# Performance work log

Measured on AMD Instinct MI355X. Metric: run time of the kernel, lower is better.

The kernel has to match this reference:

```python
import jax, jax.numpy as jnp
import numpy as np

B, N, K = 8, 1024, 1024
C1, C2 = 64, 128
EPS = 1e-5
XTOL = 1e-7


def _skew(w):
    x, y, z = w[..., 0], w[..., 1], w[..., 2]
    o = jnp.zeros_like(x)
    r0 = jnp.stack([o, -z, y], axis=-1)
    r1 = jnp.stack([z, o, -x], axis=-1)
    r2 = jnp.stack([-y, x, o], axis=-1)
    return jnp.stack([r0, r1, r2], axis=-2)


def _expmap(dx):
    # se(3) exponential map, twist = [w(3), v(3)] -> [B,4,4]
    w, v = dx[:, :3], dx[:, 3:]
    t = jnp.linalg.norm(w, axis=1)
    W = _skew(w)
    S = jnp.matmul(W, W)
    t2 = t * t
    small = t < 1e-4
    ts = jnp.where(small, jnp.ones_like(t), t)
    s1 = jnp.where(small, 1.0 - t2 / 6.0, jnp.sin(ts) / ts)            # sin(t)/t
    s2 = jnp.where(small, 0.5 - t2 / 24.0, (1.0 - jnp.cos(ts)) / (ts * ts))  # (1-cos t)/t^2
    s3 = jnp.where(small, 1.0 / 6.0 - t2 / 120.0, (ts - jnp.sin(ts)) / (ts * ts * ts))  # (t-sin t)/t^3
    I = jnp.eye(3, dtype=dx.dtype)
    R = I + s1[:, None, None] * W + s2[:, None, None] * S
    V = I + s2[:, None, None] * W + s3[:, None, None] * S
    p = jnp.einsum('bij,bj->bi', V, v)
    g = jnp.zeros((dx.shape[0], 4, 4), dtype=dx.dtype)
    g = g.at[:, :3, :3].set(R).at[:, :3, 3].set(p).at[:, 3, 3].set(1.0)
    return g


def _transform(g, p):
    # g: [B,4,4] rigid transforms, p: [B,N,3]
    return jnp.einsum('bij,bnj->bni', g[:, :3, :3], p) + g[:, None, :3, 3]


def _bn_eval(x, gamma, beta, rm, rv_):
    # eval-mode batchnorm over channel dim of [B,C,N]
    return gamma[:, None] * (x - rm[:, None]) * jax.lax.rsqrt(rv_[:, None] + EPS) + beta[:, None]


def _pointnet(p, params, with_jac=False):
    # shared-MLP PointNet: conv1x1 -> BN(eval) -> ReLU (x3), then max-pool over points
    x = jnp.swapaxes(p, 1, 2)  # [B,3,N]
    masks = []
    for (Wt, b, gamma, beta, rm, rv_) in params:
        x = jnp.einsum('oc,bcn->bon', Wt, x) + b[:, None]
        x = _bn_eval(x, gamma, beta, rm, rv_)
        x = jnp.maximum(x, 0.0)
        if with_jac:
            masks.append((x > 0.0).astype(x.dtype))
    f = jnp.max(x, axis=-1)  # [B,K]
    if with_jac:
        return f, masks, jnp.argmax(x, axis=-1)  # max_idx [B,K]
    return f


def _cal_pinv(p0, params, masks, max_idx):
    # analytical Jacobian (Cal_Jac) + Gauss-Newton pseudo-inverse
    bsz, npts = p0.shape[0], p0.shape[1]
    W1, W2, W3 = params[0][0], params[1][0], params[2][0]
    d1 = params[0][2] * jax.lax.rsqrt(params[0][5] + EPS)  # dBN/dx in eval mode (per channel)
    d2 = params[1][2] * jax.lax.rsqrt(params[1][5] + EPS)
    d3 = params[2][2] * jax.lax.rsqrt(params[2][5] + EPS)
    D1 = d1[None, :, None] * masks[0]  # [B,C1,N]
    D2 = d2[None, :, None] * masks[1]  # [B,C2,N]
    D3 = d3[None, :, None] * masks[2]  # [B,K,N]
    # feature jacobian chain d f / d p : [B,K,N,3]
    t1 = jnp.einsum('ci,bcn->bnic', W1, D1)            # [B,N,3,C1]
    t2 = jnp.einsum('bnic,dc,bdn->bnid', t1, W2, D2)   # [B,N,3,C2]
    fj = jnp.einsum('bnid,kd,bkn->bkni', t2, W3, D3)   # [B,K,N,3]
    # warp jacobian at identity twist: [-[p]x | -I3] -> [B,N,3,6]
    eye3 = jnp.broadcast_to(jnp.eye(3, dtype=p0.dtype), (bsz, npts, 3, 3))
    warp = jnp.concatenate([-_skew(p0), -eye3], axis=-1)
    # gather the argmax point per feature channel (only rows surviving max-pool)
    fjg = jnp.take_along_axis(fj, max_idx[:, :, None, None], axis=2)[:, :, 0, :]  # [B,K,3]
    wg = jnp.take_along_axis(warp.reshape(bsz, npts, 18), max_idx[:, :, None], axis=1)
    wg = wg.reshape(bsz, -1, 3, 6)  # [B,K,3,6]
    J = jnp.einsum('bki,bkim->bkm', fjg, wg)  # [B,K,6]
    H = jnp.einsum('bki,bkj->bij', J, J)      # [B,6,6]
    pinv = jnp.einsum('bij,bkj->bik', jnp.linalg.inv(H), J)  # [B,6,K]
    return pinv


def _forward(p0, p1, W1, b1, gamma1, beta1, rm1, rv1, W2, b2, gamma2, beta2, rm2, rv2, W3, b3, gamma3, beta3, rm3, rv3, maxiter):
    params = [(W1, b1, gamma1, beta1, rm1, rv1),
              (W2, b2, gamma2, beta2, rm2, rv2),
              (W3, b3, gamma3, beta3, rm3, rv3)]
    f0, masks, max_idx = _pointnet(p0, params, with_jac=True)
    pinv = _cal_pinv(p0, params, masks, max_idx)
    bsz = p0.shape[0]
    g0 = jnp.broadcast_to(jnp.eye(4, dtype=p0.dtype), (bsz, 4, 4))

    def step(carry, _):
        g, r, done = carry
        p = _transform(g, p1)
        f = _pointnet(p, params)
        r_new = jnp.where(done, r, f - f0)           # freeze residual after xtol break
        dx = jnp.einsum('bik,bk->bi', pinv, r_new)   # Gauss-Newton step [B,6]
        conv = jnp.max(jnp.linalg.norm(dx, axis=1)) < XTOL
        stop = done | conv
        g_new = jnp.where(stop, g, jnp.matmul(_expmap(dx), g))
        return (g_new, r_new, stop), None

    init = (g0, jnp.zeros_like(f0), jnp.array(False))
    (g, r, _), _ = jax.lax.scan(step, init, None, length=maxiter)
    return r


def setup_inputs():
    key = jax.random.key(0)
    ks = jax.random.split(key, 24)
    f32 = jnp.float32
    rn = lambda i, s, sc=1.0: jax.random.normal(ks[i], s, dtype=f32) * sc
    ru = lambda i, s: jax.random.uniform(ks[i], s, dtype=f32, minval=0.5, maxval=1.5)
    p0 = rn(0, (B, N, 3))
    inp = {
        'p0': p0,
        'p1': p0 + rn(1, (B, N, 3), 0.02),  # small rigid-ish perturbation -> meaningful registration
        'W1': rn(2, (C1, 3), 0.5), 'b1': rn(3, (C1,), 0.1),
        'gamma1': ru(4, (C1,)), 'beta1': rn(5, (C1,), 0.1),
        'rm1': rn(6, (C1,), 0.1), 'rv1': ru(7, (C1,)),
        'W2': rn(8, (C2, C1), 0.2), 'b2': rn(9, (C2,), 0.1),
        'gamma2': ru(10, (C2,)), 'beta2': rn(11, (C2,), 0.1),
        'rm2': rn(12, (C2,), 0.1), 'rv2': ru(13, (C2,)),
        'W3': rn(14, (K, C2), 0.1), 'b3': rn(15, (K,), 0.1),
        'gamma3': ru(16, (K,)), 'beta3': rn(17, (K,), 0.1),
        'rm3': rn(18, (K,), 0.1), 'rv3': ru(19, (K,)),
        'maxiter': 10,
    }
    return inp


def reference(p0, p1, W1, b1, gamma1, beta1, rm1, rv1, W2, b2, gamma2, beta2, rm2, rv2, W3, b3, gamma3, beta3, rm3, rv3, maxiter):
    return _forward(p0, p1, W1, b1, gamma1, beta1, rm1, rv1, W2, b2, gamma2, beta2, rm2, rv2, W3, b3, gamma3, beta3, rm3, rv3, maxiter)
```

## Files before the change

### kernel.cpp

```cpp
#include <hip/hip_runtime.h>

#define B_ 8
#define N_ 1024
#define C1_ 64
#define C2_ 128
#define K_ 1024
#define EPS_ 1e-5f
#define XTOL_ 1e-7f

#define OFF_G      0
#define OFF_F0     128
#define OFF_PM     8320
#define OFF_M1     24704
#define OFF_M2     41088
#define OFF_SC3    73856
#define OFF_OFF3   74880
#define OFF_OFF2   75904
#define OFF_W1F    76032
#define OFF_W3HI   76288
#define OFF_W3LO   141824
#define OFF_W2H    207360
#define OFF_W2L    211456
#define OFF_J      215552
#define OFF_PINVT  264704
#define OFF_PART   330240

typedef __attribute__((ext_vector_type(8))) short bf16x8;
typedef __attribute__((ext_vector_type(4))) float f32x4;

static __device__ inline unsigned short f2bf(float x) {
    unsigned u = __float_as_uint(x);
    unsigned r = (u + 0x7FFFu + ((u >> 16) & 1u)) >> 16;
    return (unsigned short)r;
}
static __device__ inline float bf2f(unsigned short h) {
    return __uint_as_float(((unsigned)h) << 16);
}
static __device__ inline unsigned pk2(unsigned short a, unsigned short b) {
    return (unsigned)a | ((unsigned)b << 16);
}

__global__ __launch_bounds__(256)
void k_prep(const float* __restrict__ W3, const float* __restrict__ b3,
            const float* __restrict__ ga3, const float* __restrict__ be3,
            const float* __restrict__ rm3, const float* __restrict__ rv3,
            const float* __restrict__ W1, const float* __restrict__ b1,
            const float* __restrict__ ga1, const float* __restrict__ be1,
            const float* __restrict__ rm1, const float* __restrict__ rv1,
            const float* __restrict__ W2, const float* __restrict__ b2,
            const float* __restrict__ ga2, const float* __restrict__ be2,
            const float* __restrict__ rm2, const float* __restrict__ rv2,
            unsigned short* __restrict__ w3hi, unsigned short* __restrict__ w3lo,
            float* __restrict__ sc3, float* __restrict__ off3,
            unsigned short* __restrict__ w2h, unsigned short* __restrict__ w2l,
            float* __restrict__ off2, float* __restrict__ w1f) {
    int gid = blockIdx.x * 256 + threadIdx.x;
    if (gid < K_ * C2_) {
        float w = W3[gid];
        unsigned short h = f2bf(w);
        w3hi[gid] = h;
        w3lo[gid] = f2bf(w - bf2f(h));
    }
    if (gid < K_) {
        float sc = ga3[gid] * rsqrtf(rv3[gid] + EPS_);
        sc3[gid] = sc;
        off3[gid] = sc * (b3[gid] - rm3[gid]) + be3[gid];
    }
    if (gid < C2_ * C1_) {
        int o = gid >> 6, c = gid & 63;
        float sc = ga2[o] * rsqrtf(rv2[o] + EPS_);
        float v = W2[o * C1_ + c] * sc;
        unsigned short h = f2bf(v);
        w2h[o * C1_ + c] = h;
        w2l[o * C1_ + c] = f2bf(v - bf2f(h));
    }
    if (gid < C2_) {
        float sc = ga2[gid] * rsqrtf(rv2[gid] + EPS_);
        off2[gid] = sc * (b2[gid] - rm2[gid]) + be2[gid];
    }
    if (gid < C1_) {
        float sc = ga1[gid] * rsqrtf(rv1[gid] + EPS_);
        w1f[gid * 4 + 0] = W1[gid * 3 + 0] * sc;
        w1f[gid * 4 + 1] = W1[gid * 3 + 1] * sc;
        w1f[gid * 4 + 2] = W1[gid * 3 + 2] * sc;
        w1f[gid * 4 + 3] = sc * (b1[gid] - rm1[gid]) + be1[gid];
    }
}

template<int MODE>
__global__ __launch_bounds__(512, 2)
void k_fused(const float* __restrict__ pts, const float* __restrict__ g,
             const float* __restrict__ w1f,
             const unsigned short* __restrict__ w2h, const unsigned short* __restrict__ w2l,
             const float* __restrict__ off2,
             const unsigned short* __restrict__ w3hi, const unsigned short* __restrict__ w3lo,
             const float* __restrict__ sc3, const float* __restrict__ off3,
             unsigned long long* __restrict__ part,
             unsigned long long* __restrict__ m1b, unsigned int* __restrict__ m2q) {
    __shared__ __align__(16) unsigned short a1h[128][72];
    __shared__ __align__(16) unsigned short a1l[128][72];
    __shared__ __align__(16) unsigned short sB[2][128][136];
    __shared__ float sSc[256], sOff[256], sOff2[C2_];
    __shared__ unsigned int m1w[2][128];
    __shared__ unsigned int m2w[4][128];
    __shared__ unsigned long long pmL[256];

    int slab = blockIdx.x;
    int b    = blockIdx.y;
    int q    = blockIdx.z;
    int n0   = slab * 128;
    int tx   = threadIdx.x;
    int w    = tx >> 6;
    int l    = tx & 63;
    int l15  = l & 15;
    int lhi  = l >> 4;

    if (tx < 256) { sSc[tx] = sc3[q * 256 + tx]; sOff[tx] = off3[q * 256 + tx]; }
    if (tx < C2_) sOff2[tx] = off2[tx];
    if (MODE == 0 && tx < 128) {
        m1w[0][tx] = 0u; m1w[1][tx] = 0u;
        m2w[0][tx] = 0u; m2w[1][tx] = 0u; m2w[2][tx] = 0u; m2w[3][tx] = 0u;
    }
    __syncthreads();

    {
        int n = tx & 127;
        int cgi = tx >> 7;
        const float* pp = pts + (b * N_ + n0 + n) * 3;
        float px = pp[0], py = pp[1], pz = pp[2];
        float q0, q1, q2;
        if (MODE == 1) {
            const float* gb = g + b * 16;
            q0 = fmaf(gb[0], px, fmaf(gb[1], py, fmaf(gb[2],  pz, gb[3])));
            q1 = fmaf(gb[4], px, fmaf(gb[5], py, fmaf(gb[6],  pz, gb[7])));
            q2 = fmaf(gb[8], px, fmaf(gb[9], py, fmaf(gb[10], pz, gb[11])));
        } else {
            q0 = px; q1 = py; q2 = pz;
        }
        unsigned int bits = 0u;
        unsigned hw[8], lw[8];
        #pragma unroll
        for (int j = 0; j < 16; ++j) {
            int c = cgi * 16 + j;
            float4 wf = *(const float4*)(w1f + c * 4);
            float y = fmaxf(fmaf(wf.x, q0, fmaf(wf.y, q1, fmaf(wf.z, q2, wf.w))), 0.f);
            unsigned short h = f2bf(y);
            unsigned short lo = f2bf(y - bf2f(h));
            if (j & 1) { hw[j >> 1] |= ((unsigned)h) << 16; lw[j >> 1] |= ((unsigned)lo) << 16; }
            else       { hw[j >> 1] = (unsigned)h;          lw[j >> 1] = (unsigned)lo; }
            if (MODE == 0) bits |= ((unsigned int)(y > 0.f)) << j;
        }
        uint4 v0; v0.x = hw[0]; v0.y = hw[1]; v0.z = hw[2]; v0.w = hw[3];
        uint4 v1; v1.x = hw[4]; v1.y = hw[5]; v1.z = hw[6]; v1.w = hw[7];
        *(uint4*)&a1h[n][cgi * 16 + 0] = v0;
        *(uint4*)&a1h[n][cgi * 16 + 8] = v1;
        uint4 v2; v2.x = lw[0]; v2.y = lw[1]; v2.z = lw[2]; v2.w = lw[3];
        uint4 v3; v3.x = lw[4]; v3.y = lw[5]; v3.z = lw[6]; v3.w = lw[7];
        *(uint4*)&a1l[n][cgi * 16 + 0] = v2;
        *(uint4*)&a1l[n][cgi * 16 + 8] = v3;
        if (MODE == 0) atomicOr(&m1w[cgi >> 1][n], bits << ((cgi & 1) * 16));
    }
    __syncthreads();

    {
        f32x4 acc2[8];
        #pragma unroll
        for (int nf = 0; nf < 8; ++nf) acc2[nf] = (f32x4){0.f, 0.f, 0.f, 0.f};
        #pragma unroll
        for (int ks = 0; ks < 2; ++ks) {
            int k0 = ks * 32;
            int aoff = (w * 16 + l15) * C1_ + k0 + lhi * 8;
            bf16x8 ah2 = *(const bf16x8*)(w2h + aoff);
            bf16x8 al2 = *(const bf16x8*)(w2l + aoff);
            #pragma unroll
            for (int nf = 0; nf < 8; ++nf) {
                bf16x8 bh2 = *(const bf16x8*)&a1h[nf * 16 + l15][k0 + lhi * 8];
                bf16x8 bl2 = *(const bf16x8*)&a1l[nf * 16 + l15][k0 + lhi * 8];
                acc2[nf] = __builtin_amdgcn_mfma_f32_16x16x32_bf16(ah2, bh2, acc2[nf], 0, 0, 0);
                acc2[nf] = __builtin_amdgcn_mfma_f32_16x16x32_bf16(ah2, bl2, acc2[nf], 0, 0, 0);
                acc2[nf] = __builtin_amdgcn_mfma_f32_16x16x32_bf16(al2, bh2, acc2[nf], 0, 0, 0);
            }
        }
        #pragma unroll
        for (int nf = 0; nf < 8; ++nf) {
            int n = nf * 16 + l15;
            unsigned short h4[4], l4[4];
            #pragma unroll
            for (int r = 0; r < 4; ++r) {
                int o = w * 16 + lhi * 4 + r;
                float y = fmaxf(acc2[nf][r] + sOff2[o], 0.f);
                unsigned short h = f2bf(y);
                h4[r] = h;
                l4[r] = f2bf(y - bf2f(h));
                if (MODE == 0 && y > 0.f) atomicOr(&m2w[o >> 5][n], 1u << (o & 31));
            }
            uint2 vh; vh.x = pk2(h4[0], h4[1]); vh.y = pk2(h4[2], h4[3]);
            uint2 vl; vl.x = pk2(l4[0], l4[1]); vl.y = pk2(l4[2], l4[3]);
            *(uint2*)&sB[0][n][w * 16 + lhi * 4] = vh;
            *(uint2*)&sB[1][n][w * 16 + lhi * 4] = vl;
        }
    }
    __syncthreads();

    if (MODE == 0 && q == 0 && tx < 128) {
        m1b[b * N_ + n0 + tx] =
            (unsigned long long)m1w[0][tx] | ((unsigned long long)m1w[1][tx] << 32);
        uint4 mv; mv.x = m2w[0][tx]; mv.y = m2w[1][tx]; mv.z = m2w[2][tx]; mv.w = m2w[3][tx];
        *(uint4*)&m2q[(b * N_ + n0 + tx) * 4] = mv;
    }

    f32x4 acc[2][8];
    #pragma unroll
    for (int fi = 0; fi < 2; ++fi)
        #pragma unroll
        for (int nf = 0; nf < 8; ++nf) acc[fi][nf] = (f32x4){0.f, 0.f, 0.f, 0.f};

    #pragma unroll
    for (int ks = 0; ks < 4; ++ks) {
        int k0 = ks * 32;
        bf16x8 bh[8], bl[8];
        #pragma unroll
        for (int nf = 0; nf < 8; ++nf) {
            bh[nf] = *(const bf16x8*)&sB[0][nf * 16 + l15][k0 + lhi * 8];
            bl[nf] = *(const bf16x8*)&sB[1][nf * 16 + l15][k0 + lhi * 8];
        }
        #pragma unroll
        for (int fi = 0; fi < 2; ++fi) {
            int orow = q * 256 + w * 32 + fi * 16 + l15;
            int off = orow * C2_ + k0 + lhi * 8;
            bf16x8 ah = *(const bf16x8*)(w3hi + off);
            bf16x8 al = *(const bf16x8*)(w3lo + off);
            #pragma unroll
            for (int nf = 0; nf < 8; ++nf) {
                acc[fi][nf] = __builtin_amdgcn_mfma_f32_16x16x32_bf16(ah, bh[nf], acc[fi][nf], 0, 0, 0);
                acc[fi][nf] = __builtin_amdgcn_mfma_f32_16x16x32_bf16(ah, bl[nf], acc[fi][nf], 0, 0, 0);
                acc[fi][nf] = __builtin_amdgcn_mfma_f32_16x16x32_bf16(al, bh[nf], acc[fi][nf], 0, 0, 0);
            }
        }
    }

    #pragma unroll
    for (int fi = 0; fi < 2; ++fi) {
        #pragma unroll
        for (int r = 0; r < 4; ++r) {
            int o_l = w * 32 + fi * 16 + lhi * 4 + r;
            float sc = sSc[o_l], of = sOff[o_l];
            float bv = -3.4e38f;
            int bi = 0;
            #pragma unroll
            for (int nf = 0; nf < 8; ++nf) {
                float y = fmaxf(sc * acc[fi][nf][r] + of, 0.f);
                int nn = n0 + nf * 16 + l15;
                if (y > bv) { bv = y; bi = nn; }
            }
            #pragma unroll
            for (int m = 1; m <= 8; m <<= 1) {
                float ov = __shfl_xor(bv, m);
                int oi = __shfl_xor(bi, m);
                if (ov > bv || (ov == bv && oi < bi)) { bv = ov; bi = oi; }
            }
            if (l15 == 0) {
                pmL[o_l] = ((unsigned long long)__float_as_uint(bv) << 32)
                         | (unsigned int)(~(unsigned int)bi);
            }
        }
    }
    __syncthreads();
    if (tx < 256)
        part[(size_t)slab * (B_ * K_) + b * K_ + q * 256 + tx] = pmL[tx];
}

__global__ __launch_bounds__(256)
void k_reduce(const unsigned long long* __restrict__ part,
              unsigned long long* __restrict__ pm) {
    int gid = blockIdx.x * 256 + threadIdx.x;
    unsigned long long m = part[gid];
    #pragma unroll
    for (int s = 1; s < 8; ++s) {
        unsigned long long v = part[(size_t)s * (B_ * K_) + gid];
        m = (v > m) ? v : m;
    }
    pm[gid] = m;
}

__global__ void k_dxupd(const unsigned long long* __restrict__ pm,
                        const float* __restrict__ f0,
                        const float* __restrict__ pinvT,
                        float* __restrict__ out, float* __restrict__ g) {
    __shared__ float dxs[B_][6];
    __shared__ float nrm[B_];
    __shared__ int sconv;
    int tx = threadIdx.x;
    int w = tx >> 6;
    int l = tx & 63;
    float acc[6] = {0.f, 0.f, 0.f, 0.f, 0.f, 0.f};
    for (int kk = l; kk < K_; kk += 64) {
        unsigned long long pk = pm[w * K_ + kk];
        float fv = __uint_as_float((unsigned int)(pk >> 32));
        float rv_ = fv - f0[w * K_ + kk];
        out[w * K_ + kk] = rv_;
        const float4* pp = (const float4*)(pinvT + (w * K_ + kk) * 8);
        float4 pa = pp[0], pb = pp[1];
        acc[0] += pa.x * rv_; acc[1] += pa.y * rv_; acc[2] += pa.z * rv_;
        acc[3] += pa.w * rv_; acc[4] += pb.x * rv_; acc[5] += pb.y * rv_;
    }
    #pragma unroll
    for (int i = 0; i < 6; ++i)
        for (int off = 32; off > 0; off >>= 1) acc[i] += __shfl_down(acc[i], off);
    if (l == 0) {
        #pragma unroll
        for (int i = 0; i < 6; ++i) dxs[w][i] = acc[i];
        nrm[w] = sqrtf(acc[0]*acc[0] + acc[1]*acc[1] + acc[2]*acc[2]
                     + acc[3]*acc[3] + acc[4]*acc[4] + acc[5]*acc[5]);
    }
    __syncthreads();
    if (tx == 0) {
        float m = nrm[0];
        for (int i = 1; i < B_; ++i) m = fmaxf(m, nrm[i]);
        sconv = (m < XTOL_) ? 1 : 0;
    }
    __syncthreads();
    if (sconv) return;
    if (l == 0) {
        float wx = dxs[w][0], wy = dxs[w][1], wz = dxs[w][2];
        float vx = dxs[w][3], vy = dxs[w][4], vz = dxs[w][5];
        float t2 = wx*wx + wy*wy + wz*wz;
        float t = sqrtf(t2);
        float s1, s2, s3;
        if (t < 1e-4f) {
            s1 = 1.f - t2 / 6.f;
            s2 = 0.5f - t2 / 24.f;
            s3 = 1.f / 6.f - t2 / 120.f;
        } else {
            float st = sinf(t), ct = cosf(t);
            s1 = st / t;
            s2 = (1.f - ct) / t2;
            s3 = (t - st) / (t2 * t);
        }
        float W[3][3] = {{0.f, -wz, wy}, {wz, 0.f, -wx}, {-wy, wx, 0.f}};
        float S[3][3];
        #pragma unroll
        for (int i = 0; i < 3; ++i)
            #pragma unroll
            for (int j = 0; j < 3; ++j)
                S[i][j] = W[i][0]*W[0][j] + W[i][1]*W[1][j] + W[i][2]*W[2][j];
        float R[3][3], V[3][3];
        #pragma unroll
        for (int i = 0; i < 3; ++i)
            #pragma unroll
            for (int j = 0; j < 3; ++j) {
                float id = (i == j) ? 1.f : 0.f;
                R[i][j] = id + s1 * W[i][j] + s2 * S[i][j];
                V[i][j] = id + s2 * W[i][j] + s3 * S[i][j];
            }
        float p[3];
        #pragma unroll
        for (int i = 0; i < 3; ++i) p[i] = V[i][0]*vx + V[i][1]*vy + V[i][2]*vz;
        float* gb = g + w * 16;
        float go[16];
        #pragma unroll
        for (int i = 0; i < 16; ++i) go[i] = gb[i];
        #pragma unroll
        for (int i = 0; i < 3; ++i)
            #pragma unroll
            for (int j = 0; j < 4; ++j)
                gb[i * 4 + j] = R[i][0]*go[0*4+j] + R[i][1]*go[1*4+j]
                              + R[i][2]*go[2*4+j] + p[i]*go[3*4+j];
    }
}

__global__ __launch_bounds__(256)
void k_jac(const float* __restrict__ p0,
           const unsigned long long* __restrict__ m1b,
           const unsigned int* __restrict__ m2q,
           const float* __restrict__ W1, const float* __restrict__ ga1, const float* __restrict__ rv1,
           const float* __restrict__ W2, const float* __restrict__ ga2, const float* __restrict__ rv2,
           const float* __restrict__ W3, const float* __restrict__ ga3, const float* __restrict__ rv3,
           const unsigned long long* __restrict__ pm,
           float* __restrict__ f0, float* __restrict__ J) {
    __shared__ float wvs[4][128];
    int tx = threadIdx.x;
    int wv = tx >> 6;
    int l = tx & 63;
    int w = blockIdx.x * 4 + wv;
    int b = w >> 10;
    int k = w & 1023;

    unsigned long long pk = pm[b * K_ + k];
    float f0v = __uint_as_float((unsigned int)(pk >> 32));
    int ns = (int)(~(unsigned int)pk);
    if (l == 0) f0[b * K_ + k] = f0v;

    unsigned long long m1 = m1b[b * N_ + ns];
    const unsigned int* mq = m2q + (b * N_ + ns) * 4;
    unsigned int qa = mq[0], qb = mq[1], qc = mq[2], qd = mq[3];
    unsigned int blo = (l < 32) ? (qa >> l) : (qb >> (l - 32));
    unsigned int bhi = (l < 32) ? (qc >> l) : (qd >> (l - 32));

    const float* w3r = W3 + k * C2_;
    float s2a = ga2[l] * rsqrtf(rv2[l] + EPS_);
    float s2b = ga2[64 + l] * rsqrtf(rv2[64 + l] + EPS_);
    float wa = (blo & 1u) ? w3r[l] * s2a : 0.f;
    float wb = (bhi & 1u) ? w3r[64 + l] * s2b : 0.f;
    wvs[wv][l] = wa;
    wvs[wv][64 + l] = wb;
    __syncthreads();

    float v = 0.f;
    #pragma unroll 8
    for (int d = 0; d < C2_; ++d) v += wvs[wv][d] * W2[d * C1_ + l];

    float d1l = ((m1 >> l) & 1ull) ? ga1[l] * rsqrtf(rv1[l] + EPS_) : 0.f;
    float vc = v * d1l;
    float fj0 = vc * W1[l * 3 + 0];
    float fj1 = vc * W1[l * 3 + 1];
    float fj2 = vc * W1[l * 3 + 2];
    #pragma unroll
    for (int off = 32; off; off >>= 1) {
        fj0 += __shfl_xor(fj0, off);
        fj1 += __shfl_xor(fj1, off);
        fj2 += __shfl_xor(fj2, off);
    }
    if (l == 0) {
        float D3 = (f0v > 0.f) ? ga3[k] * rsqrtf(rv3[k] + EPS_) : 0.f;
        fj0 *= D3; fj1 *= D3; fj2 *= D3;
        float x = p0[(b * N_ + ns) * 3 + 0];
        float y = p0[(b * N_ + ns) * 3 + 1];
        float z = p0[(b * N_ + ns) * 3 + 2];
        float* Jr = J + (b * K_ + k) * 6;
        Jr[0] = fj1 * (-z) + fj2 * y;
        Jr[1] = fj0 * z    + fj2 * (-x);
        Jr[2] = fj0 * (-y) + fj1 * x;
        Jr[3] = -fj0;
        Jr[4] = -fj1;
        Jr[5] = -fj2;
    }
}

__global__ void k_hpinv(const float* __restrict__ J, float* __restrict__ pinvT,
                        float* __restrict__ g) {
    int b = blockIdx.x;
    int tx = threadIdx.x;
    __shared__ float red[256][22];
    __shared__ float hinv[36];

    if (tx < 16) g[b * 16 + tx] = (tx % 5 == 0) ? 1.f : 0.f;

    float h[21];
    #pragma unroll
    for (int q = 0; q < 21; ++q) h[q] = 0.f;
    for (int k = tx; k < K_; k += 256) {
        const float* Jr = J + (b * K_ + k) * 6;
        float jv[6] = {Jr[0], Jr[1], Jr[2], Jr[3], Jr[4], Jr[5]};
        int q = 0;
        #pragma unroll
        for (int i = 0; i < 6; ++i)
            #pragma unroll
            for (int jj = i; jj < 6; ++jj) h[q++] += jv[i] * jv[jj];
    }
    #pragma unroll
    for (int q = 0; q < 21; ++q) red[tx][q] = h[q];
    __syncthreads();
    for (int s = 128; s > 0; s >>= 1) {
        if (tx < s)
            for (int q = 0; q < 21; ++q) red[tx][q] += red[tx + s][q];
        __syncthreads();
    }
    if (tx == 0) {
        float A[6][6], Inv[6][6];
        {
            int q = 0;
            #pragma unroll
            for (int i = 0; i < 6; ++i)
                #pragma unroll
                for (int jj = i; jj < 6; ++jj) { A[i][jj] = red[0][q]; A[jj][i] = red[0][q]; ++q; }
        }
        #pragma unroll
        for (int i = 0; i < 6; ++i)
            #pragma unroll
            for (int jj = 0; jj < 6; ++jj) Inv[i][jj] = (i == jj) ? 1.f : 0.f;
        #pragma unroll
        for (int col = 0; col < 6; ++col) {
            float ipv = 1.f / A[col][col];
            #pragma unroll
            for (int jj = 0; jj < 6; ++jj) { A[col][jj] *= ipv; Inv[col][jj] *= ipv; }
            #pragma unroll
            for (int r2 = 0; r2 < 6; ++r2) {
                if (r2 == col) continue;
                float f = A[r2][col];
                #pragma unroll
                for (int jj = 0; jj < 6; ++jj) {
                    A[r2][jj]   -= f * A[col][jj];
                    Inv[r2][jj] -= f * Inv[col][jj];
                }
            }
        }
        #pragma unroll
        for (int i = 0; i < 6; ++i)
            #pragma unroll
            for (int jj = 0; jj < 6; ++jj) hinv[i * 6 + jj] = Inv[i][jj];
    }
    __syncthreads();
    for (int k = tx; k < K_; k += 256) {
        const float* Jr = J + (b * K_ + k) * 6;
        float j0 = Jr[0], j1 = Jr[1], j2 = Jr[2], j3 = Jr[3], j4 = Jr[4], j5 = Jr[5];
        float* pr = pinvT + (b * K_ + k) * 8;
        #pragma unroll
        for (int i = 0; i < 6; ++i) {
            pr[i] = hinv[i * 6 + 0] * j0 + hinv[i * 6 + 1] * j1 + hinv[i * 6 + 2] * j2
                  + hinv[i * 6 + 3] * j3 + hinv[i * 6 + 4] * j4 + hinv[i * 6 + 5] * j5;
        }
        pr[6] = 0.f; pr[7] = 0.f;
    }
}

extern "C" void kernel_launch(void* const* d_in, const int* in_sizes, int n_in,
                              void* d_out, int out_size, void* d_ws, size_t ws_size,
                              hipStream_t stream) {
    const float* p0  = (const float*)d_in[0];
    const float* p1  = (const float*)d_in[1];
    const float* W1  = (const float*)d_in[2];
    const float* b1  = (const float*)d_in[3];
    const float* ga1 = (const float*)d_in[4];
    const float* be1 = (const float*)d_in[5];
    const float* rm1 = (const float*)d_in[6];
    const float* rv1 = (const float*)d_in[7];
    const float* W2  = (const float*)d_in[8];
    const float* b2  = (const float*)d_in[9];
    const float* ga2 = (const float*)d_in[10];
    const float* be2 = (const float*)d_in[11];
    const float* rm2 = (const float*)d_in[12];
    const float* rv2 = (const float*)d_in[13];
    const float* W3  = (const float*)d_in[14];
    const float* b3  = (const float*)d_in[15];
    const float* ga3 = (const float*)d_in[16];
    const float* be3 = (const float*)d_in[17];
    const float* rm3 = (const float*)d_in[18];
    const float* rv3 = (const float*)d_in[19];

    float* ws   = (float*)d_ws;
    float* g    = ws + OFF_G;
    float* f0   = ws + OFF_F0;
    unsigned long long* pm  = (unsigned long long*)(ws + OFF_PM);
    unsigned long long* m1b = (unsigned long long*)(ws + OFF_M1);
    unsigned int*       m2q = (unsigned int*)(ws + OFF_M2);
    float* sc3  = ws + OFF_SC3;
    float* off3 = ws + OFF_OFF3;
    float* off2 = ws + OFF_OFF2;
    float* w1f  = ws + OFF_W1F;
    unsigned short* w3hi = (unsigned short*)(ws + OFF_W3HI);
    unsigned short* w3lo = (unsigned short*)(ws + OFF_W3LO);
    unsigned short* w2h  = (unsigned short*)(ws + OFF_W2H);
    unsigned short* w2l  = (unsigned short*)(ws + OFF_W2L);
    float* Jb    = ws + OFF_J;
    float* pinvT = ws + OFF_PINVT;
    unsigned long long* part = (unsigned long long*)(ws + OFF_PART);
    float* out   = (float*)d_out;

    dim3 gridF(8, B_, 4);

    k_prep<<<(K_ * C2_ + 255) / 256, 256, 0, stream>>>(
        W3, b3, ga3, be3, rm3, rv3,
        W1, b1, ga1, be1, rm1, rv1,
        W2, b2, ga2, be2, rm2, rv2,
        w3hi, w3lo, sc3, off3, w2h, w2l, off2, w1f);

    k_fused<0><<<gridF, 512, 0, stream>>>(p0, g, w1f, w2h, w2l, off2, w3hi, w3lo,
                                          sc3, off3, part, m1b, m2q);
    k_reduce<<<B_ * K_ / 256, 256, 0, stream>>>(part, pm);
    k_jac<<<B_ * K_ / 4, 256, 0, stream>>>(p0, m1b, m2q, W1, ga1, rv1, W2, ga2, rv2,
                                           W3, ga3, rv3, pm, f0, Jb);
    k_hpinv<<<B_, 256, 0, stream>>>(Jb, pinvT, g);

    for (int it = 0; it < 10; ++it) {
        k_fused<1><<<gridF, 512, 0, stream>>>(p1, g, w1f, w2h, w2l, off2, w3hi, w3lo,
                                              sc3, off3, part, m1b, m2q);
        k_reduce<<<B_ * K_ / 256, 256, 0, stream>>>(part, pm);
        k_dxupd<<<1, 512, 0, stream>>>(pm, f0, pinvT, out, g);
    }
}
```

Before: 292.0 us.

## Fuse partial-max reduction and dx update into one kernel with last-block pattern

Inside the iteration loop, the separate partial-max reduce kernel and the single-block dx/pose update kernel are replaced by one kernel with one block per batch. Each block reduces the 8 slabs of partial maxima, computes residuals and its 6-element dx, and publishes them via atomics. The last block to arrive, chosen with an atomic counter, runs the convergence check and updates all poses. This removes one launch per iteration and the round-trip through pm, and spreads the residual work over 8 blocks. It relies on threadfence and atomic-counter ordering for correctness.

```diff
diff --git a/kernel.cpp b/kernel.cpp
--- a/kernel.cpp
+++ b/kernel.cpp
@@ -24,6 +24,9 @@
 #define OFF_J      215552
 #define OFF_PINVT  264704
 #define OFF_PART   330240
+#define OFF_DXG    461312
+#define OFF_NRM    461360
+#define OFF_CNT    461368
 
 typedef __attribute__((ext_vector_type(8))) short bf16x8;
 typedef __attribute__((ext_vector_type(4))) float f32x4;
@@ -53,7 +56,8 @@
             unsigned short* __restrict__ w3hi, unsigned short* __restrict__ w3lo,
             float* __restrict__ sc3, float* __restrict__ off3,
             unsigned short* __restrict__ w2h, unsigned short* __restrict__ w2l,
-            float* __restrict__ off2, float* __restrict__ w1f) {
+            float* __restrict__ off2, float* __restrict__ w1f,
+            unsigned int* __restrict__ cnt) {
     int gid = blockIdx.x * 256 + threadIdx.x;
     if (gid < K_ * C2_) {
         float w = W3[gid];
@@ -85,6 +89,7 @@
         w1f[gid * 4 + 2] = W1[gid * 3 + 2] * sc;
         w1f[gid * 4 + 3] = sc * (b1[gid] - rm1[gid]) + be1[gid];
     }
+    if (gid == 0) *cnt = 0u;
 }
 
 template<int MODE>
@@ -283,47 +288,77 @@
     pm[gid] = m;
 }
 
-__global__ void k_dxupd(const unsigned long long* __restrict__ pm,
-                        const float* __restrict__ f0,
-                        const float* __restrict__ pinvT,
-                        float* __restrict__ out, float* __restrict__ g) {
-    __shared__ float dxs[B_][6];
-    __shared__ float nrm[B_];
-    __shared__ int sconv;
+__global__ __launch_bounds__(256)
+void k_rdx(const unsigned long long* __restrict__ part,
+           const float* __restrict__ f0, const float* __restrict__ pinvT,
+           float* __restrict__ out, float* __restrict__ g,
+           float* __restrict__ dxg, float* __restrict__ nrmg,
+           unsigned int* __restrict__ cnt) {
+    __shared__ float redB[4][6];
+    __shared__ int isLast;
+    int bb = blockIdx.x;
     int tx = threadIdx.x;
     int w = tx >> 6;
     int l = tx & 63;
+
     float acc[6] = {0.f, 0.f, 0.f, 0.f, 0.f, 0.f};
-    for (int kk = l; kk < K_; kk += 64) {
-        unsigned long long pk = pm[w * K_ + kk];
-        float fv = __uint_as_float((unsigned int)(pk >> 32));
-        float rv_ = fv - f0[w * K_ + kk];
-        out[w * K_ + kk] = rv_;
-        const float4* pp = (const float4*)(pinvT + (w * K_ + kk) * 8);
+    #pragma unroll
+    for (int half = 0; half < 4; ++half) {
+        int o = half * 256 + tx;
+        unsigned long long m = part[(size_t)bb * K_ + o];
+        #pragma unroll
+        for (int s = 1; s < 8; ++s) {
+            unsigned long long v = part[(size_t)s * (B_ * K_) + bb * K_ + o];
+            m = (v > m) ? v : m;
+        }
+        float fv = __uint_as_float((unsigned int)(m >> 32));
+        float rv = fv - f0[bb * K_ + o];
+        out[bb * K_ + o] = rv;
+        const float4* pp = (const float4*)(pinvT + (size_t)(bb * K_ + o) * 8);
         float4 pa = pp[0], pb = pp[1];
-        acc[0] += pa.x * rv_; acc[1] += pa.y * rv_; acc[2] += pa.z * rv_;
-        acc[3] += pa.w * rv_; acc[4] += pb.x * rv_; acc[5] += pb.y * rv_;
+        acc[0] += pa.x * rv; acc[1] += pa.y * rv; acc[2] += pa.z * rv;
+        acc[3] += pa.w * rv; acc[4] += pb.x * rv; acc[5] += pb.y * rv;
     }
     #pragma unroll
     for (int i = 0; i < 6; ++i)
         for (int off = 32; off > 0; off >>= 1) acc[i] += __shfl_down(acc[i], off);
     if (l == 0) {
         #pragma unroll
-        for (int i = 0; i < 6; ++i) dxs[w][i] = acc[i];
-        nrm[w] = sqrtf(acc[0]*acc[0] + acc[1]*acc[1] + acc[2]*acc[2]
-                     + acc[3]*acc[3] + acc[4]*acc[4] + acc[5]*acc[5]);
+        for (int i = 0; i < 6; ++i) redB[w][i] = acc[i];
     }
     __syncthreads();
     if (tx == 0) {
-        float m = nrm[0];
-        for (int i = 1; i < B_; ++i) m = fmaxf(m, nrm[i]);
-        sconv = (m < XTOL_) ? 1 : 0;
-    }
-    __syncthreads();
-    if (sconv) return;
-    if (l == 0) {
-        float wx = dxs[w][0], wy = dxs[w][1], wz = dxs[w][2];
-        float vx = dxs[w][3], vy = dxs[w][4], vz = dxs[w][5];
+        float dx6[6];
+        #pragma unroll
+        for (int i = 0; i < 6; ++i) {
+            dx6[i] = redB[0][i] + redB[1][i] + redB[2][i] + redB[3][i];
+            atomicExch(&dxg[bb * 6 + i], dx6[i]);
+        }
+        atomicExch(&nrmg[bb],
+                   sqrtf(dx6[0]*dx6[0] + dx6[1]*dx6[1] + dx6[2]*dx6[2]
+                       + dx6[3]*dx6[3] + dx6[4]*dx6[4] + dx6[5]*dx6[5]));
+    }
+    __threadfence();
+    __syncthreads();
+    if (tx == 0) {
+        unsigned int old = atomicAdd(cnt, 1u);
+        isLast = (old == B_ - 1) ? 1 : 0;
+        if (isLast) atomicExch(cnt, 0u);
+    }
+    __syncthreads();
+    if (!isLast) return;
+
+    if (tx < B_) {
+        int b = tx;
+        float mx = 0.f;
+        #pragma unroll
+        for (int i = 0; i < B_; ++i) mx = fmaxf(mx, atomicAdd(&nrmg[i], 0.f));
+        if (mx < XTOL_) return;
+        float d[6];
+        #pragma unroll
+        for (int i = 0; i < 6; ++i) d[i] = atomicAdd(&dxg[b * 6 + i], 0.f);
+        float wx = d[0], wy = d[1], wz = d[2];
+        float vx = d[3], vy = d[4], vz = d[5];
         float t2 = wx*wx + wy*wy + wz*wz;
         float t = sqrtf(t2);
         float s1, s2, s3;
@@ -356,7 +391,7 @@
         float p[3];
         #pragma unroll
         for (int i = 0; i < 3; ++i) p[i] = V[i][0]*vx + V[i][1]*vy + V[i][2]*vz;
-        float* gb = g + w * 16;
+        float* gb = g + b * 16;
         float go[16];
         #pragma unroll
         for (int i = 0; i < 16; ++i) go[i] = gb[i];
@@ -555,6 +590,9 @@
     float* Jb    = ws + OFF_J;
     float* pinvT = ws + OFF_PINVT;
     unsigned long long* part = (unsigned long long*)(ws + OFF_PART);
+    float* dxg   = ws + OFF_DXG;
+    float* nrmg  = ws + OFF_NRM;
+    unsigned int* cnt = (unsigned int*)(ws + OFF_CNT);
     float* out   = (float*)d_out;
 
     dim3 gridF(8, B_, 4);
@@ -563,7 +601,7 @@
         W3, b3, ga3, be3, rm3, rv3,
         W1, b1, ga1, be1, rm1, rv1,
         W2, b2, ga2, be2, rm2, rv2,
-        w3hi, w3lo, sc3, off3, w2h, w2l, off2, w1f);
+        w3hi, w3lo, sc3, off3, w2h, w2l, off2, w1f, cnt);
 
     k_fused<0><<<gridF, 512, 0, stream>>>(p0, g, w1f, w2h, w2l, off2, w3hi, w3lo,
                                           sc3, off3, part, m1b, m2q);
@@ -575,7 +613,6 @@
     for (int it = 0; it < 10; ++it) {
         k_fused<1><<<gridF, 512, 0, stream>>>(p1, g, w1f, w2h, w2l, off2, w3hi, w3lo,
                                               sc3, off3, part, m1b, m2q);
-        k_reduce<<<B_ * K_ / 256, 256, 0, stream>>>(part, pm);
-        k_dxupd<<<1, 512, 0, stream>>>(pm, f0, pinvT, out, g);
-    }
-}
+        k_rdx<<<B_, 256, 0, stream>>>(part, f0, pinvT, out, g, dxg, nrmg, cnt);
+    }
+}
```

Result: faster. 277.6 us (-4.9%).
